# Optimization experiments

Measured on AMD Instinct MI355X. Metric: run time of the kernel, lower is better.

The kernel has to match this reference:

```python
import jax, jax.numpy as jnp
import numpy as np

N, E, F_IN, HID, EPS = 50000, 800000, 128, 256, 1e-5

def _glorot(key, shape):
    scale = 1.0 / np.sqrt(shape[0])
    return jax.random.uniform(key, shape, jnp.float32, -scale, scale)

def setup_inputs() -> dict:
    key = jax.random.key(0)
    ks = jax.random.split(key, 20)
    x = jax.random.normal(ks[0], (N, F_IN), jnp.float32)
    edge_index = jax.random.randint(ks[1], (2, E), 0, N, jnp.int64)
    inp = {"x": x, "edge_index": edge_index}
    dims = [F_IN, HID, HID]
    for i in range(3):
        d_in = dims[i]
        inp[f"Wn{i}"] = _glorot(ks[2 + 4 * i], (d_in, HID))      # lin_l weight (neighbors), with bias
        inp[f"bn{i}"] = jnp.zeros((HID,), jnp.float32)
        inp[f"Wr{i}"] = _glorot(ks[3 + 4 * i], (d_in, HID))      # lin_r weight (root), no bias
        inp[f"g{i}"] = jnp.ones((HID,), jnp.float32)              # BN gamma
        inp[f"b{i}"] = jnp.zeros((HID,), jnp.float32)             # BN beta
    return inp

def _sage_bn_elu(x, src, dst, Wn, bn, Wr, g, b):
    # mean aggregation of source features onto destination nodes
    agg = jax.ops.segment_sum(x[src], dst, num_segments=N)                      # [N, d_in]
    deg = jax.ops.segment_sum(jnp.ones((src.shape[0],), x.dtype), dst, num_segments=N)
    agg = agg / jnp.maximum(deg, 1.0)[:, None]
    h = agg @ Wn + bn + x @ Wr                                                  # SAGEConv(root_weight=True)
    mu = jnp.mean(h, axis=0)
    var = jnp.mean((h - mu) ** 2, axis=0)                                       # biased var (BN training)
    h = (h - mu) * jax.lax.rsqrt(var + EPS) * g + b
    return jnp.where(h > 0, h, jnp.expm1(h))                                    # ELU(alpha=1)

def reference(x, edge_index, Wn0, bn0, Wr0, g0, b0, Wn1, bn1, Wr1, g1, b1, Wn2, bn2, Wr2, g2, b2):
    src, dst = edge_index[0], edge_index[1]
    h = _sage_bn_elu(x, src, dst, Wn0, bn0, Wr0, g0, b0)
    h = _sage_bn_elu(h, src, dst, Wn1, bn1, Wr1, g1, b1)
    h = _sage_bn_elu(h, src, dst, Wn2, bn2, Wr2, g2, b2)
    return h
```

## Files before the change

### kernel.cpp

```cpp
#include <hip/hip_runtime.h>
#include <math.h>

#define N_NODES 50000
#define N_EDGES 800000
#define F_IN    128
#define HID     256
#define BN_EPS  1e-5f
#define SCAN_BLOCKS ((N_NODES + 255) / 256)
#define ROW_BLOCKS  ((N_NODES + 127) / 128)

typedef unsigned int uint;
typedef __attribute__((ext_vector_type(8))) short bf16x8;
typedef __attribute__((ext_vector_type(4))) float f32x4;

__device__ __forceinline__ float bf2f(unsigned short u) {
    return __uint_as_float((uint)u << 16);
}
__device__ __forceinline__ unsigned short f2bf(float f) {
    uint u = __float_as_uint(f);
    return (unsigned short)((u + 0x7FFFu + ((u >> 16) & 1u)) >> 16);
}

__device__ __forceinline__ void gload16(const unsigned short* g, unsigned short* l) {
    __builtin_amdgcn_global_load_lds(
        (const __attribute__((address_space(1))) void*)g,
        (__attribute__((address_space(3))) void*)l, 16, 0, 0);
}

__global__ void hist_kernel(const int* __restrict__ dst, int* __restrict__ deg) {
    int e = blockIdx.x * blockDim.x + threadIdx.x;
    if (e < N_EDGES) atomicAdd(&deg[dst[e]], 1);
}

__global__ __launch_bounds__(256) void scan1_kernel(const int* __restrict__ deg,
                                                    int* __restrict__ row_ptr,
                                                    int* __restrict__ partials) {
    __shared__ int sm[256];
    int i = blockIdx.x * 256 + threadIdx.x;
    int v = (i < N_NODES) ? deg[i] : 0;
    sm[threadIdx.x] = v;
    __syncthreads();
    for (int off = 1; off < 256; off <<= 1) {
        int t = (threadIdx.x >= off) ? sm[threadIdx.x - off] : 0;
        __syncthreads();
        sm[threadIdx.x] += t;
        __syncthreads();
    }
    if (i < N_NODES) row_ptr[i] = sm[threadIdx.x] - v;
    if (threadIdx.x == 255) partials[blockIdx.x] = sm[255];
}

__global__ __launch_bounds__(256) void scan2_kernel(int* __restrict__ partials) {
    __shared__ int sm[256];
    int t = threadIdx.x;
    int v = (t < SCAN_BLOCKS) ? partials[t] : 0;
    sm[t] = v;
    __syncthreads();
    for (int off = 1; off < 256; off <<= 1) {
        int p = (t >= off) ? sm[t - off] : 0;
        __syncthreads();
        sm[t] += p;
        __syncthreads();
    }
    if (t < SCAN_BLOCKS) partials[t] = sm[t] - v;
}

__global__ __launch_bounds__(256) void scan3_kernel(int* __restrict__ row_ptr,
                                                    int* __restrict__ cursor,
                                                    const int* __restrict__ partials) {
    int i = blockIdx.x * 256 + threadIdx.x;
    if (i < N_NODES) {
        int v = row_ptr[i] + partials[blockIdx.x];
        row_ptr[i] = v;
        cursor[i]  = v;
    }
    if (i == 0) row_ptr[N_NODES] = N_EDGES;
}

__global__ void fill_kernel(const int* __restrict__ src, const int* __restrict__ dst,
                            int* __restrict__ cursor, int* __restrict__ csr_src) {
    int e = blockIdx.x * blockDim.x + threadIdx.x;
    if (e >= N_EDGES) return;
    int pos = atomicAdd(&cursor[dst[e]], 1);
    csr_src[pos] = src[e];
}

__global__ void cast_bf16_kernel(const float* __restrict__ x, unsigned short* __restrict__ xb,
                                 int total4) {
    int i = blockIdx.x * blockDim.x + threadIdx.x;
    if (i >= total4) return;
    float4 v = *(const float4*)&x[(long)i * 4];
    unsigned short o[4] = {f2bf(v.x), f2bf(v.y), f2bf(v.z), f2bf(v.w)};
    *(uint2*)&xb[(long)i * 4] = *(const uint2*)o;
}

__global__ __launch_bounds__(256) void wt_kernel(const float* __restrict__ Wn,
                                                 const float* __restrict__ Wr,
                                                 int K1, int KT, unsigned short* __restrict__ WT) {
    int n  = threadIdx.x;
    int k0 = blockIdx.x * 16;
    unsigned short o[16];
#pragma unroll
    for (int j = 0; j < 16; ++j) {
        int k = k0 + j;
        float v = (k < K1) ? Wn[k * HID + n] : Wr[(k - K1) * HID + n];
        o[j] = f2bf(v);
    }
    *(uint4*)&WT[(long)n * KT + k0]     = *(const uint4*)&o[0];
    *(uint4*)&WT[(long)n * KT + k0 + 8] = *(const uint4*)&o[8];
}

template<int D>
__global__ __launch_bounds__(256) void gather_mean_kernel(
    const unsigned short* __restrict__ x, const int* __restrict__ row_ptr,
    const int* __restrict__ csr_src, unsigned short* __restrict__ agg) {
    constexpr int VPL = D / 64;
    int node = blockIdx.x * 4 + (threadIdx.x >> 6);
    int lane = threadIdx.x & 63;
    if (node >= N_NODES) return;
    int beg = row_ptr[node], end = row_ptr[node + 1];
    float acc[VPL];
#pragma unroll
    for (int j = 0; j < VPL; j++) acc[j] = 0.f;
    int e = beg;
    for (; e + 4 <= end; e += 4) {
        int s0 = csr_src[e], s1 = csr_src[e + 1], s2 = csr_src[e + 2], s3 = csr_src[e + 3];
        if constexpr (VPL == 4) {
            uint2 v0 = *(const uint2*)&x[(long)s0 * D + lane * 4];
            uint2 v1 = *(const uint2*)&x[(long)s1 * D + lane * 4];
            uint2 v2 = *(const uint2*)&x[(long)s2 * D + lane * 4];
            uint2 v3 = *(const uint2*)&x[(long)s3 * D + lane * 4];
            acc[0] += (bf2f((unsigned short)(v0.x & 0xFFFF)) + bf2f((unsigned short)(v1.x & 0xFFFF)))
                    + (bf2f((unsigned short)(v2.x & 0xFFFF)) + bf2f((unsigned short)(v3.x & 0xFFFF)));
            acc[1] += (bf2f((unsigned short)(v0.x >> 16))    + bf2f((unsigned short)(v1.x >> 16)))
                    + (bf2f((unsigned short)(v2.x >> 16))    + bf2f((unsigned short)(v3.x >> 16)));
            acc[2] += (bf2f((unsigned short)(v0.y & 0xFFFF)) + bf2f((unsigned short)(v1.y & 0xFFFF)))
                    + (bf2f((unsigned short)(v2.y & 0xFFFF)) + bf2f((unsigned short)(v3.y & 0xFFFF)));
            acc[3] += (bf2f((unsigned short)(v0.y >> 16))    + bf2f((unsigned short)(v1.y >> 16)))
                    + (bf2f((unsigned short)(v2.y >> 16))    + bf2f((unsigned short)(v3.y >> 16)));
        } else {
            uint v0 = *(const uint*)&x[(long)s0 * D + lane * 2];
            uint v1 = *(const uint*)&x[(long)s1 * D + lane * 2];
            uint v2 = *(const uint*)&x[(long)s2 * D + lane * 2];
            uint v3 = *(const uint*)&x[(long)s3 * D + lane * 2];
            acc[0] += (bf2f((unsigned short)(v0 & 0xFFFF)) + bf2f((unsigned short)(v1 & 0xFFFF)))
                    + (bf2f((unsigned short)(v2 & 0xFFFF)) + bf2f((unsigned short)(v3 & 0xFFFF)));
            acc[1] += (bf2f((unsigned short)(v0 >> 16))    + bf2f((unsigned short)(v1 >> 16)))
                    + (bf2f((unsigned short)(v2 >> 16))    + bf2f((unsigned short)(v3 >> 16)));
        }
    }
    for (; e < end; e++) {
        int s0 = csr_src[e];
        if constexpr (VPL == 4) {
            uint2 v0 = *(const uint2*)&x[(long)s0 * D + lane * 4];
            acc[0] += bf2f((unsigned short)(v0.x & 0xFFFF));
            acc[1] += bf2f((unsigned short)(v0.x >> 16));
            acc[2] += bf2f((unsigned short)(v0.y & 0xFFFF));
            acc[3] += bf2f((unsigned short)(v0.y >> 16));
        } else {
            uint v0 = *(const uint*)&x[(long)s0 * D + lane * 2];
            acc[0] += bf2f((unsigned short)(v0 & 0xFFFF));
            acc[1] += bf2f((unsigned short)(v0 >> 16));
        }
    }
    float inv = 1.0f / fmaxf((float)(end - beg), 1.0f);
    unsigned short* o = &agg[(long)node * D + lane * VPL];
    if constexpr (VPL == 4) {
        unsigned short ov[4] = {f2bf(acc[0] * inv), f2bf(acc[1] * inv),
                                f2bf(acc[2] * inv), f2bf(acc[3] * inv)};
        *(uint2*)o = *(const uint2*)ov;
    } else {
        unsigned short ov[2] = {f2bf(acc[0] * inv), f2bf(acc[1] * inv)};
        *(uint*)o = *(const uint*)ov;
    }
}

template<int K1, int K2>
__global__ __launch_bounds__(256) void mfma_gemm_kernel(
    const unsigned short* __restrict__ A1, const unsigned short* __restrict__ A2,
    const unsigned short* __restrict__ WT, const float* __restrict__ bias,
    unsigned short* __restrict__ Hout, float* __restrict__ sred) {
    constexpr int KT = K1 + K2;
    constexpr int NITER = KT / 64;
    __shared__ unsigned short As[2][128 * 64];
    __shared__ unsigned short Bs[2][128 * 64];
    __shared__ float cs[128];
    __shared__ float cq[128];

    const int tid  = threadIdx.x;
    const int wave = tid >> 6;
    const int lane = tid & 63;
    const int m16  = lane & 15;
    const int quad = lane >> 4;
    const int row_block = blockIdx.x >> 1;
    const int col_half  = blockIdx.x & 1;
    const int r0 = row_block * 128;
    const int rl = lane >> 3;
    const int cl = lane & 7;
    const int csw = cl ^ rl;

    if (tid < 128) { cs[tid] = 0.f; cq[tid] = 0.f; }

    f32x4 acc[2][8];
#pragma unroll
    for (int mt = 0; mt < 2; mt++)
#pragma unroll
        for (int nt = 0; nt < 8; nt++) acc[mt][nt] = (f32x4){0.f, 0.f, 0.f, 0.f};

    auto issue = [&](int t) {
        const int buf = t & 1;
        const int k0  = t * 64;
        const unsigned short* Ab;
        int pitch, kk;
        if (k0 < K1) { Ab = A1; pitch = K1; kk = k0; }
        else         { Ab = A2; pitch = K2; kk = k0 - K1; }
#pragma unroll
        for (int j = 0; j < 4; ++j) {
            int lr = wave * 32 + j * 8 + rl;
            long gr = min(r0 + lr, N_NODES - 1);
            gload16(&Ab[gr * pitch + kk + csw * 8], &As[buf][(wave * 32 + j * 8) * 64]);
        }
#pragma unroll
        for (int j = 0; j < 4; ++j) {
            int lr = wave * 32 + j * 8 + rl;
            long gn = col_half * 128 + lr;
            gload16(&WT[gn * KT + k0 + csw * 8], &Bs[buf][(wave * 32 + j * 8) * 64]);
        }
    };

    issue(0);

#pragma unroll
    for (int it = 0; it < NITER; ++it) {
        const int cur = it & 1;
        if (it + 1 < NITER) {
            issue(it + 1);
            asm volatile("s_waitcnt vmcnt(8)" ::: "memory");
        } else {
            asm volatile("s_waitcnt vmcnt(0)" ::: "memory");
        }
        __builtin_amdgcn_s_barrier();
#pragma unroll
        for (int ks = 0; ks < 2; ++ks) {
            bf16x8 afrag[2], bfrag[8];
#pragma unroll
            for (int mt = 0; mt < 2; mt++) {
                int ar = wave * 32 + mt * 16 + m16;
                afrag[mt] = *(const bf16x8*)&As[cur][ar * 64 + (((ks * 4 + quad) ^ (m16 & 7)) * 8)];
            }
#pragma unroll
            for (int nt = 0; nt < 8; nt++) {
                int br = nt * 16 + m16;
                bfrag[nt] = *(const bf16x8*)&Bs[cur][br * 64 + (((ks * 4 + quad) ^ (m16 & 7)) * 8)];
            }
#pragma unroll
            for (int mt = 0; mt < 2; mt++)
#pragma unroll
                for (int nt = 0; nt < 8; nt++)
                    acc[mt][nt] = __builtin_amdgcn_mfma_f32_16x16x32_bf16(
                        afrag[mt], bfrag[nt], acc[mt][nt], 0, 0, 0);
        }
        __builtin_amdgcn_s_barrier();
    }

#pragma unroll
    for (int nt = 0; nt < 8; nt++) {
        int lcol = nt * 16 + m16;
        int col  = col_half * 128 + lcol;
        float bv = bias[col];
        float s = 0.f, q = 0.f;
#pragma unroll
        for (int mt = 0; mt < 2; mt++) {
#pragma unroll
            for (int reg = 0; reg < 4; reg++) {
                int row = r0 + wave * 32 + mt * 16 + quad * 4 + reg;
                float v = acc[mt][nt][reg] + bv;
                if (row < N_NODES) {
                    Hout[(long)row * HID + col] = f2bf(v);
                    s += v;
                    q += v * v;
                }
            }
        }
        s += __shfl_xor(s, 16); s += __shfl_xor(s, 32);
        q += __shfl_xor(q, 16); q += __shfl_xor(q, 32);
        if (quad == 0) {
            atomicAdd(&cs[lcol], s);
            atomicAdd(&cq[lcol], q);
        }
    }
    __syncthreads();
    if (tid < 128) {
        sred[(long)blockIdx.x * 256 + tid]       = cs[tid];
        sred[(long)blockIdx.x * 256 + 128 + tid] = cq[tid];
    }
}

__global__ __launch_bounds__(256) void bn_reduce_kernel(const float* __restrict__ sred,
                                                        const float* __restrict__ g,
                                                        const float* __restrict__ b,
                                                        float* __restrict__ ss) {
    int t  = threadIdx.x;
    int hf = t >> 7;
    int lc = t & 127;
    float S[4] = {0.f, 0.f, 0.f, 0.f}, Q[4] = {0.f, 0.f, 0.f, 0.f};
    int rb = 0;
    for (; rb + 4 <= ROW_BLOCKS; rb += 4) {
#pragma unroll
        for (int u = 0; u < 4; u++) {
            const float* p = &sred[(long)((rb + u) * 2 + hf) * 256 + lc];
            S[u] += p[0];
            Q[u] += p[128];
        }
    }
    for (; rb < ROW_BLOCKS; rb++) {
        const float* p = &sred[(long)(rb * 2 + hf) * 256 + lc];
        S[0] += p[0];
        Q[0] += p[128];
    }
    float Sv = (S[0] + S[1]) + (S[2] + S[3]);
    float Qv = (Q[0] + Q[1]) + (Q[2] + Q[3]);
    float mu  = Sv * (1.0f / N_NODES);
    float var = Qv * (1.0f / N_NODES) - mu * mu;
    var = fmaxf(var, 0.f);
    float sc = rsqrtf(var + BN_EPS) * g[t];
    ss[t]       = sc;
    ss[HID + t] = b[t] - mu * sc;
}

template<bool OUT32>
__global__ void bn_elu_kernel(const unsigned short* __restrict__ h, const float* __restrict__ ss,
                              void* __restrict__ out) {
    const int total4 = N_NODES * HID / 4;
    int i = blockIdx.x * blockDim.x + threadIdx.x;
    if (i >= total4) return;
    int c4 = (i % (HID / 4)) * 4;
    uint2 v = *(const uint2*)&h[(long)i * 4];
    float4 sc = *(const float4*)&ss[c4];
    float4 sh = *(const float4*)&ss[HID + c4];
    float in[4] = {bf2f((unsigned short)(v.x & 0xFFFF)), bf2f((unsigned short)(v.x >> 16)),
                   bf2f((unsigned short)(v.y & 0xFFFF)), bf2f((unsigned short)(v.y >> 16))};
    float scv[4] = {sc.x, sc.y, sc.z, sc.w};
    float shv[4] = {sh.x, sh.y, sh.z, sh.w};
    float o[4];
#pragma unroll
    for (int j = 0; j < 4; j++) {
        float t = fmaf(in[j], scv[j], shv[j]);
        o[j] = t > 0.f ? t : expm1f(t);
    }
    if (OUT32) {
        float4 ov = {o[0], o[1], o[2], o[3]};
        *(float4*)&((float*)out)[(long)i * 4] = ov;
    } else {
        unsigned short ov[4] = {f2bf(o[0]), f2bf(o[1]), f2bf(o[2]), f2bf(o[3])};
        *(uint2*)&((unsigned short*)out)[(long)i * 4] = *(const uint2*)ov;
    }
}

extern "C" void kernel_launch(void* const* d_in, const int* in_sizes, int n_in,
                              void* d_out, int out_size, void* d_ws, size_t ws_size,
                              hipStream_t stream) {
    const float* x   = (const float*)d_in[0];
    const int*   ei  = (const int*)d_in[1];
    const int*   src = ei;
    const int*   dst = ei + N_EDGES;
    const float* Wn[3] = {(const float*)d_in[2],  (const float*)d_in[7],  (const float*)d_in[12]};
    const float* bn[3] = {(const float*)d_in[3],  (const float*)d_in[8],  (const float*)d_in[13]};
    const float* Wr[3] = {(const float*)d_in[4],  (const float*)d_in[9],  (const float*)d_in[14]};
    const float* g [3] = {(const float*)d_in[5],  (const float*)d_in[10], (const float*)d_in[15]};
    const float* b [3] = {(const float*)d_in[6],  (const float*)d_in[11], (const float*)d_in[16]};
    float* out = (float*)d_out;

    const size_t BF = (size_t)N_NODES * HID * 2;
    char* ws = (char*)d_ws;
    unsigned short* B0  = (unsigned short*)(ws);
    unsigned short* B1  = (unsigned short*)(ws + BF);
    unsigned short* B2  = (unsigned short*)(ws + 2 * BF);
    unsigned short* XB  = (unsigned short*)(ws + 3 * BF);
    char* ws2 = ws + 3 * BF + (size_t)N_NODES * F_IN * 2;
    unsigned short* WT0 = (unsigned short*)(ws2);
    unsigned short* WT1 = (unsigned short*)(ws2 + 256 * 256 * 2);
    unsigned short* WT2 = (unsigned short*)(ws2 + 256 * 256 * 2 + 256 * 512 * 2);
    char* ws3 = ws2 + 256 * 256 * 2 + 2 * (256 * 512 * 2);
    int*   row_ptr = (int*)ws3;
    int*   cursor  = row_ptr + (N_NODES + 1);
    int*   deg_i   = cursor + N_NODES;
    int*   partial = deg_i + N_NODES;
    int*   csr_src = partial + SCAN_BLOCKS;
    float* sred    = (float*)(csr_src + N_EDGES);
    float* ss      = sred + (size_t)ROW_BLOCKS * 2 * 256;

    const int eb = (N_EDGES + 255) / 256;
    const int gather_blocks = (N_NODES + 3) / 4;
    const int elu_blocks = (N_NODES * HID / 4 + 255) / 256;
    const int gemm_blocks = ROW_BLOCKS * 2;

    hipMemsetAsync(deg_i, 0, N_NODES * sizeof(int), stream);
    hist_kernel<<<eb, 256, 0, stream>>>(dst, deg_i);
    scan1_kernel<<<SCAN_BLOCKS, 256, 0, stream>>>(deg_i, row_ptr, partial);
    scan2_kernel<<<1, 256, 0, stream>>>(partial);
    scan3_kernel<<<SCAN_BLOCKS, 256, 0, stream>>>(row_ptr, cursor, partial);
    fill_kernel<<<eb, 256, 0, stream>>>(src, dst, cursor, csr_src);
    cast_bf16_kernel<<<(N_NODES * F_IN / 4 + 255) / 256, 256, 0, stream>>>(x, XB, N_NODES * F_IN / 4);
    wt_kernel<<<(2 * F_IN) / 16, 256, 0, stream>>>(Wn[0], Wr[0], F_IN, 2 * F_IN, WT0);
    wt_kernel<<<(2 * HID) / 16, 256, 0, stream>>>(Wn[1], Wr[1], HID, 2 * HID, WT1);
    wt_kernel<<<(2 * HID) / 16, 256, 0, stream>>>(Wn[2], Wr[2], HID, 2 * HID, WT2);

    gather_mean_kernel<F_IN><<<gather_blocks, 256, 0, stream>>>(XB, row_ptr, csr_src, B0);
    mfma_gemm_kernel<F_IN, F_IN><<<gemm_blocks, 256, 0, stream>>>(B0, XB, WT0, bn[0], B1, sred);
    bn_reduce_kernel<<<1, 256, 0, stream>>>(sred, g[0], b[0], ss);
    bn_elu_kernel<false><<<elu_blocks, 256, 0, stream>>>(B1, ss, B2);

    gather_mean_kernel<HID><<<gather_blocks, 256, 0, stream>>>(B2, row_ptr, csr_src, B0);
    mfma_gemm_kernel<HID, HID><<<gemm_blocks, 256, 0, stream>>>(B0, B2, WT1, bn[1], B1, sred);
    bn_reduce_kernel<<<1, 256, 0, stream>>>(sred, g[1], b[1], ss);
    bn_elu_kernel<false><<<elu_blocks, 256, 0, stream>>>(B1, ss, B2);

    gather_mean_kernel<HID><<<gather_blocks, 256, 0, stream>>>(B2, row_ptr, csr_src, B0);
    mfma_gemm_kernel<HID, HID><<<gemm_blocks, 256, 0, stream>>>(B0, B2, WT2, bn[2], B1, sred);
    bn_reduce_kernel<<<1, 256, 0, stream>>>(sred, g[2], b[2], ss);
    bn_elu_kernel<true><<<elu_blocks, 256, 0, stream>>>(B1, ss, out);
}
```

Before: 566.8 us.

## Widen gather loads to 16B with split-edge lanes; enlarge GEMM tile to 256x256

```diff
diff --git a/kernel.cpp b/kernel.cpp
--- a/kernel.cpp
+++ b/kernel.cpp
@@ -7,7 +7,7 @@
 #define HID     256
 #define BN_EPS  1e-5f
 #define SCAN_BLOCKS ((N_NODES + 255) / 256)
-#define ROW_BLOCKS  ((N_NODES + 127) / 128)
+#define RB256       ((N_NODES + 255) / 256)
 
 typedef unsigned int uint;
 typedef __attribute__((ext_vector_type(8))) short bf16x8;
@@ -25,6 +25,19 @@
     __builtin_amdgcn_global_load_lds(
         (const __attribute__((address_space(1))) void*)g,
         (__attribute__((address_space(3))) void*)l, 16, 0, 0);
+}
+
+__device__ __forceinline__ void acc_u4(float* a, uint4 v) {
+    a[0] += bf2f((unsigned short)(v.x & 0xFFFF)); a[1] += bf2f((unsigned short)(v.x >> 16));
+    a[2] += bf2f((unsigned short)(v.y & 0xFFFF)); a[3] += bf2f((unsigned short)(v.y >> 16));
+    a[4] += bf2f((unsigned short)(v.z & 0xFFFF)); a[5] += bf2f((unsigned short)(v.z >> 16));
+    a[6] += bf2f((unsigned short)(v.w & 0xFFFF)); a[7] += bf2f((unsigned short)(v.w >> 16));
+}
+__device__ __forceinline__ void acc_u4m(float* a, uint4 v, float m) {
+    a[0] += m * bf2f((unsigned short)(v.x & 0xFFFF)); a[1] += m * bf2f((unsigned short)(v.x >> 16));
+    a[2] += m * bf2f((unsigned short)(v.y & 0xFFFF)); a[3] += m * bf2f((unsigned short)(v.y >> 16));
+    a[4] += m * bf2f((unsigned short)(v.z & 0xFFFF)); a[5] += m * bf2f((unsigned short)(v.z >> 16));
+    a[6] += m * bf2f((unsigned short)(v.w & 0xFFFF)); a[7] += m * bf2f((unsigned short)(v.w >> 16));
 }
 
 __global__ void hist_kernel(const int* __restrict__ dst, int* __restrict__ deg) {
@@ -114,98 +127,107 @@
 __global__ __launch_bounds__(256) void gather_mean_kernel(
     const unsigned short* __restrict__ x, const int* __restrict__ row_ptr,
     const int* __restrict__ csr_src, unsigned short* __restrict__ agg) {
-    constexpr int VPL = D / 64;
     int node = blockIdx.x * 4 + (threadIdx.x >> 6);
     int lane = threadIdx.x & 63;
     if (node >= N_NODES) return;
     int beg = row_ptr[node], end = row_ptr[node + 1];
-    float acc[VPL];
-#pragma unroll
-    for (int j = 0; j < VPL; j++) acc[j] = 0.f;
+    float acc[8];
+#pragma unroll
+    for (int j = 0; j < 8; j++) acc[j] = 0.f;
     int e = beg;
-    for (; e + 4 <= end; e += 4) {
-        int s0 = csr_src[e], s1 = csr_src[e + 1], s2 = csr_src[e + 2], s3 = csr_src[e + 3];
-        if constexpr (VPL == 4) {
-            uint2 v0 = *(const uint2*)&x[(long)s0 * D + lane * 4];
-            uint2 v1 = *(const uint2*)&x[(long)s1 * D + lane * 4];
-            uint2 v2 = *(const uint2*)&x[(long)s2 * D + lane * 4];
-            uint2 v3 = *(const uint2*)&x[(long)s3 * D + lane * 4];
-            acc[0] += (bf2f((unsigned short)(v0.x & 0xFFFF)) + bf2f((unsigned short)(v1.x & 0xFFFF)))
-                    + (bf2f((unsigned short)(v2.x & 0xFFFF)) + bf2f((unsigned short)(v3.x & 0xFFFF)));
-            acc[1] += (bf2f((unsigned short)(v0.x >> 16))    + bf2f((unsigned short)(v1.x >> 16)))
-                    + (bf2f((unsigned short)(v2.x >> 16))    + bf2f((unsigned short)(v3.x >> 16)));
-            acc[2] += (bf2f((unsigned short)(v0.y & 0xFFFF)) + bf2f((unsigned short)(v1.y & 0xFFFF)))
-                    + (bf2f((unsigned short)(v2.y & 0xFFFF)) + bf2f((unsigned short)(v3.y & 0xFFFF)));
-            acc[3] += (bf2f((unsigned short)(v0.y >> 16))    + bf2f((unsigned short)(v1.y >> 16)))
-                    + (bf2f((unsigned short)(v2.y >> 16))    + bf2f((unsigned short)(v3.y >> 16)));
-        } else {
-            uint v0 = *(const uint*)&x[(long)s0 * D + lane * 2];
-            uint v1 = *(const uint*)&x[(long)s1 * D + lane * 2];
-            uint v2 = *(const uint*)&x[(long)s2 * D + lane * 2];
-            uint v3 = *(const uint*)&x[(long)s3 * D + lane * 2];
-            acc[0] += (bf2f((unsigned short)(v0 & 0xFFFF)) + bf2f((unsigned short)(v1 & 0xFFFF)))
-                    + (bf2f((unsigned short)(v2 & 0xFFFF)) + bf2f((unsigned short)(v3 & 0xFFFF)));
-            acc[1] += (bf2f((unsigned short)(v0 >> 16))    + bf2f((unsigned short)(v1 >> 16)))
-                    + (bf2f((unsigned short)(v2 >> 16))    + bf2f((unsigned short)(v3 >> 16)));
-        }
-    }
-    for (; e < end; e++) {
-        int s0 = csr_src[e];
-        if constexpr (VPL == 4) {
-            uint2 v0 = *(const uint2*)&x[(long)s0 * D + lane * 4];
-            acc[0] += bf2f((unsigned short)(v0.x & 0xFFFF));
-            acc[1] += bf2f((unsigned short)(v0.x >> 16));
-            acc[2] += bf2f((unsigned short)(v0.y & 0xFFFF));
-            acc[3] += bf2f((unsigned short)(v0.y >> 16));
-        } else {
-            uint v0 = *(const uint*)&x[(long)s0 * D + lane * 2];
-            acc[0] += bf2f((unsigned short)(v0 & 0xFFFF));
-            acc[1] += bf2f((unsigned short)(v0 >> 16));
-        }
-    }
-    float inv = 1.0f / fmaxf((float)(end - beg), 1.0f);
-    unsigned short* o = &agg[(long)node * D + lane * VPL];
-    if constexpr (VPL == 4) {
-        unsigned short ov[4] = {f2bf(acc[0] * inv), f2bf(acc[1] * inv),
-                                f2bf(acc[2] * inv), f2bf(acc[3] * inv)};
-        *(uint2*)o = *(const uint2*)ov;
+
+    if constexpr (D == 256) {
+        const int half = lane >> 5;
+        const long lo  = (long)(lane & 31) * 8;
+        for (; e + 8 <= end; e += 8) {
+            int s0 = csr_src[e + half],     s1 = csr_src[e + 2 + half];
+            int s2 = csr_src[e + 4 + half], s3 = csr_src[e + 6 + half];
+            uint4 v0 = *(const uint4*)&x[(long)s0 * 256 + lo];
+            uint4 v1 = *(const uint4*)&x[(long)s1 * 256 + lo];
+            uint4 v2 = *(const uint4*)&x[(long)s2 * 256 + lo];
+            uint4 v3 = *(const uint4*)&x[(long)s3 * 256 + lo];
+            acc_u4(acc, v0); acc_u4(acc, v1); acc_u4(acc, v2); acc_u4(acc, v3);
+        }
+        for (; e + 2 <= end; e += 2) {
+            int s0 = csr_src[e + half];
+            uint4 v0 = *(const uint4*)&x[(long)s0 * 256 + lo];
+            acc_u4(acc, v0);
+        }
+        if (e < end) {
+            int s0 = csr_src[e];
+            uint4 v0 = *(const uint4*)&x[(long)s0 * 256 + lo];
+            acc_u4m(acc, v0, (half == 0) ? 1.f : 0.f);
+        }
+#pragma unroll
+        for (int j = 0; j < 8; j++) acc[j] += __shfl_xor(acc[j], 32);
+        float inv = 1.0f / fmaxf((float)(end - beg), 1.0f);
+        if (half == 0) {
+            unsigned short ov[8];
+#pragma unroll
+            for (int j = 0; j < 8; j++) ov[j] = f2bf(acc[j] * inv);
+            *(uint4*)&agg[(long)node * 256 + lo] = *(const uint4*)ov;
+        }
     } else {
-        unsigned short ov[2] = {f2bf(acc[0] * inv), f2bf(acc[1] * inv)};
-        *(uint*)o = *(const uint*)ov;
+        const int grp = lane >> 4;
+        const long lo = (long)(lane & 15) * 8;
+        for (; e + 8 <= end; e += 8) {
+            int sA = csr_src[e + grp], sB = csr_src[e + 4 + grp];
+            uint4 vA = *(const uint4*)&x[(long)sA * 128 + lo];
+            uint4 vB = *(const uint4*)&x[(long)sB * 128 + lo];
+            acc_u4(acc, vA); acc_u4(acc, vB);
+        }
+        for (; e + 4 <= end; e += 4) {
+            int sA = csr_src[e + grp];
+            uint4 vA = *(const uint4*)&x[(long)sA * 128 + lo];
+            acc_u4(acc, vA);
+        }
+        for (; e < end; e++) {
+            int s0 = csr_src[e];
+            uint4 v0 = *(const uint4*)&x[(long)s0 * 128 + lo];
+            acc_u4m(acc, v0, (grp == 0) ? 1.f : 0.f);
+        }
+#pragma unroll
+        for (int j = 0; j < 8; j++) {
+            acc[j] += __shfl_xor(acc[j], 32);
+            acc[j] += __shfl_xor(acc[j], 16);
+        }
+        float inv = 1.0f / fmaxf((float)(end - beg), 1.0f);
+        if (lane < 16) {
+            unsigned short ov[8];
+#pragma unroll
+            for (int j = 0; j < 8; j++) ov[j] = f2bf(acc[j] * inv);
+            *(uint4*)&agg[(long)node * 128 + lo] = *(const uint4*)ov;
+        }
     }
 }
 
 template<int K1, int K2>
-__global__ __launch_bounds__(256) void mfma_gemm_kernel(
+__global__ __launch_bounds__(512) void mfma_gemm_kernel(
     const unsigned short* __restrict__ A1, const unsigned short* __restrict__ A2,
     const unsigned short* __restrict__ WT, const float* __restrict__ bias,
     unsigned short* __restrict__ Hout, float* __restrict__ sred) {
     constexpr int KT = K1 + K2;
     constexpr int NITER = KT / 64;
-    __shared__ unsigned short As[2][128 * 64];
-    __shared__ unsigned short Bs[2][128 * 64];
-    __shared__ float cs[128];
-    __shared__ float cq[128];
+    __shared__ unsigned short As[2][256 * 64];
+    __shared__ unsigned short Bs[2][256 * 64];
 
     const int tid  = threadIdx.x;
     const int wave = tid >> 6;
     const int lane = tid & 63;
     const int m16  = lane & 15;
     const int quad = lane >> 4;
-    const int row_block = blockIdx.x >> 1;
-    const int col_half  = blockIdx.x & 1;
-    const int r0 = row_block * 128;
+    const int WR   = wave >> 2;
+    const int WC   = wave & 3;
+    const int r0   = blockIdx.x * 256;
     const int rl = lane >> 3;
     const int cl = lane & 7;
     const int csw = cl ^ rl;
 
-    if (tid < 128) { cs[tid] = 0.f; cq[tid] = 0.f; }
-
-    f32x4 acc[2][8];
-#pragma unroll
-    for (int mt = 0; mt < 2; mt++)
-#pragma unroll
-        for (int nt = 0; nt < 8; nt++) acc[mt][nt] = (f32x4){0.f, 0.f, 0.f, 0.f};
+    f32x4 acc[8][4];
+#pragma unroll
+    for (int mt = 0; mt < 8; mt++)
+#pragma unroll
+        for (int nt = 0; nt < 4; nt++) acc[mt][nt] = (f32x4){0.f, 0.f, 0.f, 0.f};
 
     auto issue = [&](int t) {
         const int buf = t & 1;
@@ -222,8 +244,7 @@
         }
 #pragma unroll
         for (int j = 0; j < 4; ++j) {
-            int lr = wave * 32 + j * 8 + rl;
-            long gn = col_half * 128 + lr;
+            long gn = wave * 32 + j * 8 + rl;
             gload16(&WT[gn * KT + k0 + csw * 8], &Bs[buf][(wave * 32 + j * 8) * 64]);
         }
     };
@@ -242,21 +263,21 @@
         __builtin_amdgcn_s_barrier();
 #pragma unroll
         for (int ks = 0; ks < 2; ++ks) {
-            bf16x8 afrag[2], bfrag[8];
-#pragma unroll
-            for (int mt = 0; mt < 2; mt++) {
-                int ar = wave * 32 + mt * 16 + m16;
+            bf16x8 afrag[8], bfrag[4];
+#pragma unroll
+            for (int mt = 0; mt < 8; mt++) {
+                int ar = WR * 128 + mt * 16 + m16;
                 afrag[mt] = *(const bf16x8*)&As[cur][ar * 64 + (((ks * 4 + quad) ^ (m16 & 7)) * 8)];
             }
 #pragma unroll
-            for (int nt = 0; nt < 8; nt++) {
-                int br = nt * 16 + m16;
+            for (int nt = 0; nt < 4; nt++) {
+                int br = WC * 64 + nt * 16 + m16;
                 bfrag[nt] = *(const bf16x8*)&Bs[cur][br * 64 + (((ks * 4 + quad) ^ (m16 & 7)) * 8)];
             }
 #pragma unroll
-            for (int mt = 0; mt < 2; mt++)
-#pragma unroll
-                for (int nt = 0; nt < 8; nt++)
+            for (int mt = 0; mt < 8; mt++)
+#pragma unroll
+                for (int nt = 0; nt < 4; nt++)
                     acc[mt][nt] = __builtin_amdgcn_mfma_f32_16x16x32_bf16(
                         afrag[mt], bfrag[nt], acc[mt][nt], 0, 0, 0);
         }
@@ -264,19 +285,18 @@
     }
 
 #pragma unroll
-    for (int nt = 0; nt < 8; nt++) {
-        int lcol = nt * 16 + m16;
-        int col  = col_half * 128 + lcol;
-        float bv = bias[col];
+    for (int nt = 0; nt < 4; nt++) {
+        int lcol = WC * 64 + nt * 16 + m16;
+        float bv = bias[lcol];
         float s = 0.f, q = 0.f;
 #pragma unroll
-        for (int mt = 0; mt < 2; mt++) {
+        for (int mt = 0; mt < 8; mt++) {
 #pragma unroll
             for (int reg = 0; reg < 4; reg++) {
-                int row = r0 + wave * 32 + mt * 16 + quad * 4 + reg;
+                int row = r0 + WR * 128 + mt * 16 + quad * 4 + reg;
                 float v = acc[mt][nt][reg] + bv;
                 if (row < N_NODES) {
-                    Hout[(long)row * HID + col] = f2bf(v);
+                    Hout[(long)row * HID + lcol] = f2bf(v);
                     s += v;
                     q += v * v;
                 }
@@ -285,47 +305,41 @@
         s += __shfl_xor(s, 16); s += __shfl_xor(s, 32);
         q += __shfl_xor(q, 16); q += __shfl_xor(q, 32);
         if (quad == 0) {
-            atomicAdd(&cs[lcol], s);
-            atomicAdd(&cq[lcol], q);
-        }
-    }
-    __syncthreads();
-    if (tid < 128) {
-        sred[(long)blockIdx.x * 256 + tid]       = cs[tid];
-        sred[(long)blockIdx.x * 256 + 128 + tid] = cq[tid];
-    }
-}
-
-__global__ __launch_bounds__(256) void bn_reduce_kernel(const float* __restrict__ sred,
+            float* base = &sred[(long)(blockIdx.x * 2 + WR) * 512];
+            base[lcol]       = s;
+            base[256 + lcol] = q;
+        }
+    }
+}
+
+__global__ __launch_bounds__(512) void bn_reduce_kernel(const float* __restrict__ sred,
                                                         const float* __restrict__ g,
                                                         const float* __restrict__ b,
-                                                        float* __restrict__ ss) {
+                                                        float* __restrict__ ss, int nrows) {
+    __shared__ float qsm[256];
     int t  = threadIdx.x;
-    int hf = t >> 7;
-    int lc = t & 127;
-    float S[4] = {0.f, 0.f, 0.f, 0.f}, Q[4] = {0.f, 0.f, 0.f, 0.f};
+    int ch = t & 255;
+    int off = (t < 256) ? 0 : 256;
+    float S0 = 0.f, S1 = 0.f, S2 = 0.f, S3 = 0.f;
     int rb = 0;
-    for (; rb + 4 <= ROW_BLOCKS; rb += 4) {
-#pragma unroll
-        for (int u = 0; u < 4; u++) {
-            const float* p = &sred[(long)((rb + u) * 2 + hf) * 256 + lc];
-            S[u] += p[0];
-            Q[u] += p[128];
-        }
-    }
-    for (; rb < ROW_BLOCKS; rb++) {
-        const float* p = &sred[(long)(rb * 2 + hf) * 256 + lc];
-        S[0] += p[0];
-        Q[0] += p[128];
-    }
-    float Sv = (S[0] + S[1]) + (S[2] + S[3]);
-    float Qv = (Q[0] + Q[1]) + (Q[2] + Q[3]);
-    float mu  = Sv * (1.0f / N_NODES);
-    float var = Qv * (1.0f / N_NODES) - mu * mu;
-    var = fmaxf(var, 0.f);
-    float sc = rsqrtf(var + BN_EPS) * g[t];
-    ss[t]       = sc;
-    ss[HID + t] = b[t] - mu * sc;
+    for (; rb + 4 <= nrows; rb += 4) {
+        S0 += sred[(long)(rb + 0) * 512 + off + ch];
+        S1 += sred[(long)(rb + 1) * 512 + off + ch];
+        S2 += sred[(long)(rb + 2) * 512 + off + ch];
+        S3 += sred[(long)(rb + 3) * 512 + off + ch];
+    }
+    for (; rb < nrows; rb++) S0 += sred[(long)rb * 512 + off + ch];
+    float Sv = (S0 + S1) + (S2 + S3);
+    if (t >= 256) qsm[ch] = Sv;
+    __syncthreads();
+    if (t < 256) {
+        float mu  = Sv * (1.0f / N_NODES);
+        float var = qsm[ch] * (1.0f / N_NODES) - mu * mu;
+        var = fmaxf(var, 0.f);
+        float sc = rsqrtf(var + BN_EPS) * g[ch];
+        ss[ch]       = sc;
+        ss[HID + ch] = b[ch] - mu * sc;
+    }
 }
 
 template<bool OUT32>
@@ -388,12 +402,11 @@
     int*   partial = deg_i + N_NODES;
     int*   csr_src = partial + SCAN_BLOCKS;
     float* sred    = (float*)(csr_src + N_EDGES);
-    float* ss      = sred + (size_t)ROW_BLOCKS * 2 * 256;
+    float* ss      = sred + (size_t)2 * RB256 * 512;
 
     const int eb = (N_EDGES + 255) / 256;
     const int gather_blocks = (N_NODES + 3) / 4;
     const int elu_blocks = (N_NODES * HID / 4 + 255) / 256;
-    const int gemm_blocks = ROW_BLOCKS * 2;
 
     hipMemsetAsync(deg_i, 0, N_NODES * sizeof(int), stream);
     hist_kernel<<<eb, 256, 0, stream>>>(dst, deg_i);
@@ -407,17 +420,17 @@
     wt_kernel<<<(2 * HID) / 16, 256, 0, stream>>>(Wn[2], Wr[2], HID, 2 * HID, WT2);
 
     gather_mean_kernel<F_IN><<<gather_blocks, 256, 0, stream>>>(XB, row_ptr, csr_src, B0);
-    mfma_gemm_kernel<F_IN, F_IN><<<gemm_blocks, 256, 0, stream>>>(B0, XB, WT0, bn[0], B1, sred);
-    bn_reduce_kernel<<<1, 256, 0, stream>>>(sred, g[0], b[0], ss);
+    mfma_gemm_kernel<F_IN, F_IN><<<RB256, 512, 0, stream>>>(B0, XB, WT0, bn[0], B1, sred);
+    bn_reduce_kernel<<<1, 512, 0, stream>>>(sred, g[0], b[0], ss, 2 * RB256);
     bn_elu_kernel<false><<<elu_blocks, 256, 0, stream>>>(B1, ss, B2);
 
     gather_mean_kernel<HID><<<gather_blocks, 256, 0, stream>>>(B2, row_ptr, csr_src, B0);
-    mfma_gemm_kernel<HID, HID><<<gemm_blocks, 256, 0, stream>>>(B0, B2, WT1, bn[1], B1, sred);
-    bn_reduce_kernel<<<1, 256, 0, stream>>>(sred, g[1], b[1], ss);
+    mfma_gemm_kernel<HID, HID><<<RB256, 512, 0, stream>>>(B0, B2, WT1, bn[1], B1, sred);
+    bn_reduce_kernel<<<1, 512, 0, stream>>>(sred, g[1], b[1], ss, 2 * RB256);
     bn_elu_kernel<false><<<elu_blocks, 256, 0, stream>>>(B1, ss, B2);
 
     gather_mean_kernel<HID><<<gather_blocks, 256, 0, stream>>>(B2, row_ptr, csr_src, B0);
-    mfma_gemm_kernel<HID, HID><<<gemm_blocks, 256, 0, stream>>>(B0, B2, WT2, bn[2], B1, sred);
-    bn_reduce_kernel<<<1, 256, 0, stream>>>(sred, g[2], b[2], ss);
+    mfma_gemm_kernel<HID, HID><<<RB256, 512, 0, stream>>>(B0, B2, WT2, bn[2], B1, sred);
+    bn_reduce_kernel<<<1, 512, 0, stream>>>(sred, g[2], b[2], ss, 2 * RB256);
     bn_elu_kernel<true><<<elu_blocks, 256, 0, stream>>>(B1, ss, out);
 }
```

After: 578.0 us. About the same (+2.0%).
